# Kernel tuning notes

Hardware: AMD Instinct MI355X
Metric: run time of the kernel (lower is better)

Reference implementation:

```python
import jax, jax.numpy as jnp
import numpy as np
import math

N = 256  # channels == model dim M
B, H, W = 8, 48, 48
EPS = 1e-5


def _kaiming(key, shape, a=math.sqrt(5)):
    # kaiming_normal_ with fan_in = shape[1] (2D weight), leaky_relu gain
    fan_in = shape[1]
    gain = math.sqrt(2.0 / (1.0 + a * a))
    std = gain / math.sqrt(fan_in)
    return std * jax.random.normal(key, shape, dtype=jnp.float32)


def setup_inputs() -> dict:
    key = jax.random.key(0)
    ks = jax.random.split(key, 6)
    x_l = jax.random.normal(ks[0], (B, N, H, W), dtype=jnp.float32)
    x_r = jax.random.normal(ks[1], (B, N, H, W), dtype=jnp.float32)
    Wq = _kaiming(ks[2], (N, N))
    Wk = _kaiming(ks[3], (N, N))
    Wv = _kaiming(ks[4], (N, N))
    Wo = _kaiming(ks[5], (N, N))
    g1 = jnp.ones((N,), jnp.float32); b1 = jnp.zeros((N,), jnp.float32)
    g2 = jnp.ones((N,), jnp.float32); b2 = jnp.zeros((N,), jnp.float32)
    return {"x_l": x_l, "x_r": x_r, "Wq": Wq, "Wk": Wk, "Wv": Wv, "Wo": Wo,
            "g1": g1, "b1": b1, "g2": g2, "b2": b2}


def _layernorm(x, g, b):
    mu = jnp.mean(x, axis=-1, keepdims=True)
    var = jnp.mean(jnp.square(x - mu), axis=-1, keepdims=True)
    return (x - mu) * jax.lax.rsqrt(var + EPS) * g + b


def reference(x_l, x_r, Wq, Wk, Wv, Wo, g1, b1, g2, b2):
    Bsz, C, Hh, Ww = x_l.shape
    S = Hh * Ww
    # [B, C, H, W] -> [B, S, C]
    xl = x_l.reshape(Bsz, C, S).transpose(0, 2, 1)
    xr = x_r.reshape(Bsz, C, S).transpose(0, 2, 1)
    xln_l = _layernorm(xl, g1, b1)
    xln_r = _layernorm(xr, g2, b2)
    Ql = xln_l @ Wq; Qr = xln_r @ Wq
    Kl = xln_l @ Wk; Kr = xln_r @ Wk
    Vl = xln_l @ Wv; Vr = xln_r @ Wv
    scale = 1.0 / math.sqrt(C)
    Al = jnp.einsum('bsc,btc->bst', Ql, Kr) * scale  # [B,S,S]
    Ar = jnp.einsum('bsc,btc->bst', Qr, Kl) * scale
    # NOTE: original uses nn.Softmax() with dim=None; for a 3-D tensor torch's
    # legacy _get_softmax_dim resolves to dim=0 (over batch). Faithfully replicated.
    Pl = jax.nn.softmax(Al, axis=0)
    Pr = jax.nn.softmax(Ar, axis=0)
    out_l = xl + (Pl @ Vl) @ Wo
    out_r = xr + (Pr @ Vr) @ Wo
    out_l = out_l.transpose(0, 2, 1).reshape(Bsz, C, Hh, Ww)
    out_r = out_r.transpose(0, 2, 1).reshape(Bsz, C, Hh, Ww)
    return out_l, out_r
```

## Files before the change

### kernel.cpp

```cpp
#include <hip/hip_runtime.h>
#include <stdint.h>

#define SDIM 2304
#define CDIM 256
#define NB   8
#define MTOT (NB * SDIM)

typedef __attribute__((ext_vector_type(8))) short short8;
typedef __attribute__((ext_vector_type(4))) float f32x4;

__device__ __forceinline__ float b2f(unsigned short h) {
  union { unsigned int u; float f; } v; v.u = ((unsigned int)h) << 16; return v.f;
}
__device__ __forceinline__ unsigned short f2b(float f) {
  union { unsigned int u; float f; } v; v.f = f;
  unsigned int u = v.u;
  u += 0x7fffu + ((u >> 16) & 1u);
  return (unsigned short)(u >> 16);
}
static inline unsigned short f2b_host(float f) {
  union { unsigned int u; float f; } v; v.f = f;
  unsigned int u = v.u;
  u += 0x7fffu + ((u >> 16) & 1u);
  return (unsigned short)(u >> 16);
}

__device__ __forceinline__ void gload_lds16(const unsigned short* g, unsigned short* l) {
  __builtin_amdgcn_global_load_lds(
      (const __attribute__((address_space(1))) unsigned int*)g,
      (__attribute__((address_space(3))) unsigned int*)l,
      16, 0, 0);
}

__global__ __launch_bounds__(64)
void detect_dtype(const unsigned short* __restrict__ x, int* __restrict__ flag)
{
  int lane = threadIdx.x;
  int bad = 0;
  for (int i = lane; i < 1024; i += 64) {
    float v = b2f(x[i]);
    if (!(fabsf(v) < 1e20f)) bad = 1;
  }
  unsigned long long m = __ballot(bad);
  if (lane == 0) flag[0] = (m != 0ULL) ? 1 : 0;
}

constexpr int EP_PLAIN = 0, EP_QKV = 1, EP_OUT = 2, EP_ACC = 3;

template <int EP, int SW>
__global__ __launch_bounds__(256, 2)
void gemm_nt(const unsigned short* __restrict__ pA, int lda, long sAz,
             const unsigned short* __restrict__ pB, int ldb, long sBz, int zx,
             unsigned short* __restrict__ pC, int ldc, long sCz,
             unsigned short* __restrict__ pQ, unsigned short* __restrict__ pK,
             unsigned short* __restrict__ pV,
             const unsigned short* __restrict__ pX0, const unsigned short* __restrict__ pX1,
             float* __restrict__ pFacc, unsigned short* __restrict__ pBf, int accmode,
             const int* __restrict__ dflag, int Kdim)
{
  __shared__ __align__(16) unsigned short As[4][128 * 32];
  __shared__ __align__(16) unsigned short Bs[4][128 * 32];

  const int tid = threadIdx.x;
  int bx, by, bz;
  if constexpr (SW == 1) {
    const int h = blockIdx.x;
    const int q = h >> 4, r = h & 15;
    const int p = q * 8 + (r & 7);
    by = r >> 3;
    bx = p % 18;
    bz = p / 18;
  } else if constexpr (SW == 2) {
    const int b = blockIdx.x;
    const int n = (b & 7) * 648 + (b >> 3);
    bz = n / 324; const int r = n % 324; by = r / 18; bx = r % 18;
  } else {
    bx = blockIdx.x; by = blockIdx.y; bz = blockIdx.z;
  }
  const int z = bz;
  const long m0 = (long)bx * 128;
  const long n0 = (long)by * 128;
  const unsigned short* A  = pA + (long)z * sAz;
  const unsigned short* Bm = pB + (long)(z ^ zx) * sBz;

  const int lane = tid & 63;
  const int wave = tid >> 6;
  const int wm = (wave & 1) << 6;
  const int wn = (wave >> 1) << 6;
  const int lr = lane & 15;
  const int quad = lane >> 4;

  f32x4 acc[4][4];
#pragma unroll
  for (int i = 0; i < 4; ++i)
#pragma unroll
    for (int j = 0; j < 4; ++j) acc[i][j] = (f32x4)0.0f;

  const int e0 = tid, e1 = tid + 256;
  const int r0 = e0 >> 2, c0 = (((e0 & 3) ^ ((r0 >> 1) & 3)) << 3);
  const int r1 = e1 >> 2, c1 = (((e1 & 3) ^ ((r1 >> 1) & 3)) << 3);
  const unsigned short* pa0 = A  + (m0 + r0) * lda + c0;
  const unsigned short* pa1 = A  + (m0 + r1) * lda + c1;
  const unsigned short* pb0 = Bm + (n0 + r0) * ldb + c0;
  const unsigned short* pb1 = Bm + (n0 + r1) * ldb + c1;

  const int chunk = quad ^ ((lr >> 1) & 3);
  int aoff[4], boff[4];
#pragma unroll
  for (int i = 0; i < 4; ++i) {
    aoff[i] = (wm + i * 16 + lr) * 32 + chunk * 8;
    boff[i] = (wn + i * 16 + lr) * 32 + chunk * 8;
  }

  const int nt = Kdim >> 5;

  auto stage = [&](int kt) {
    const int sl = kt & 3;
    const int k = kt << 5;
    gload_lds16(pa0 + k, &As[sl][e0 * 8]);
    gload_lds16(pa1 + k, &As[sl][e1 * 8]);
    gload_lds16(pb0 + k, &Bs[sl][e0 * 8]);
    gload_lds16(pb1 + k, &Bs[sl][e1 * 8]);
  };

  stage(0); stage(1); stage(2);

  for (int t = 0; t < nt; ++t) {
    if (t < nt - 2)       asm volatile("s_waitcnt vmcnt(8)" ::: "memory");
    else if (t == nt - 2) asm volatile("s_waitcnt vmcnt(4)" ::: "memory");
    else                  asm volatile("s_waitcnt vmcnt(0)" ::: "memory");
    __builtin_amdgcn_s_barrier();
    asm volatile("" ::: "memory");

    if (t + 3 < nt) stage(t + 3);

    const int sl = t & 3;
    short8 af[4], bfr[4];
#pragma unroll
    for (int i = 0; i < 4; ++i) {
      af[i]  = *(const short8*)&As[sl][aoff[i]];
      bfr[i] = *(const short8*)&Bs[sl][boff[i]];
    }
    __builtin_amdgcn_s_setprio(1);
#pragma unroll
    for (int i = 0; i < 4; ++i)
#pragma unroll
      for (int j = 0; j < 4; ++j)
        acc[i][j] = __builtin_amdgcn_mfma_f32_16x16x32_bf16(af[i], bfr[j], acc[i][j], 0, 0, 0);
    __builtin_amdgcn_s_setprio(0);
  }

  if constexpr (EP == EP_PLAIN) {
    unsigned short* Cp = pC + (long)z * sCz;
#pragma unroll
    for (int i = 0; i < 4; ++i) {
      const long mb = m0 + wm + i * 16 + quad * 4;
#pragma unroll
      for (int j = 0; j < 4; ++j) {
        const long n = n0 + wn + j * 16 + lr;
#pragma unroll
        for (int r = 0; r < 4; ++r)
          Cp[(mb + r) * ldc + n] = f2b(acc[i][j][r]);
      }
    }
  } else if constexpr (EP == EP_QKV) {
    const int g  = (int)(n0 >> 8);
    const int nb = (int)(n0 & 255);
    if (g < 2) {
      unsigned short* Cp = (g == 0 ? pQ : pK) + (long)z * sCz;
#pragma unroll
      for (int i = 0; i < 4; ++i) {
        const long mb = m0 + wm + i * 16 + quad * 4;
#pragma unroll
        for (int j = 0; j < 4; ++j) {
          const int n = nb + wn + j * 16 + lr;
#pragma unroll
          for (int r = 0; r < 4; ++r)
            Cp[(mb + r) * CDIM + n] = f2b(acc[i][j][r]);
        }
      }
    } else {
      const int b = (int)(m0 / SDIM);
      const int sblk = (int)(m0 % SDIM);
      unsigned short* Vz = pV + ((long)z * NB + b) * (long)CDIM * SDIM;
#pragma unroll
      for (int i = 0; i < 4; ++i) {
        const int s = sblk + wm + i * 16 + quad * 4;
#pragma unroll
        for (int j = 0; j < 4; ++j) {
          const int c = nb + wn + j * 16 + lr;
          ushort4 pk;
          pk.x = f2b(acc[i][j][0]); pk.y = f2b(acc[i][j][1]);
          pk.z = f2b(acc[i][j][2]); pk.w = f2b(acc[i][j][3]);
          *(ushort4*)&Vz[(long)c * SDIM + s] = pk;
        }
      }
    }
  } else if constexpr (EP == EP_ACC) {
    float* Fz = pFacc + (long)z * SDIM * CDIM;
    unsigned short* Bz = pBf + (long)z * SDIM * CDIM;
#pragma unroll
    for (int i = 0; i < 4; ++i) {
      const long mb = m0 + wm + i * 16 + quad * 4;
#pragma unroll
      for (int j = 0; j < 4; ++j) {
        const long n = n0 + wn + j * 16 + lr;
#pragma unroll
        for (int r = 0; r < 4; ++r) {
          const long idx = (mb + r) * CDIM + n;
          float v = acc[i][j][r];
          if (accmode != 0) v += Fz[idx];
          if (accmode == 2) Bz[idx] = f2b(v);
          else              Fz[idx] = v;
        }
      }
    }
  } else {
    const int io32 = dflag[0];
    const int b = (int)(m0 / SDIM);
    const int sblk = (int)(m0 % SDIM);
    const unsigned short* Xraw = (z == 0 ? pX0 : pX1);
    if (io32) {
      const float* Xf = (const float*)Xraw + (long)b * CDIM * SDIM;
      float* Of = (float*)pC + (long)z * sCz + (long)b * CDIM * SDIM;
#pragma unroll
      for (int i = 0; i < 4; ++i) {
        const int s = sblk + wm + i * 16 + quad * 4;
#pragma unroll
        for (int j = 0; j < 4; ++j) {
          const int c = (int)n0 + wn + j * 16 + lr;
          const long off = (long)c * SDIM + s;
          float4 rx = *(const float4*)&Xf[off];
          float4 pk;
          pk.x = acc[i][j][0] + rx.x;
          pk.y = acc[i][j][1] + rx.y;
          pk.z = acc[i][j][2] + rx.z;
          pk.w = acc[i][j][3] + rx.w;
          *(float4*)&Of[off] = pk;
        }
      }
    } else {
      const unsigned short* X = Xraw + (long)b * CDIM * SDIM;
      unsigned short* O = pC + (long)z * sCz + (long)b * CDIM * SDIM;
#pragma unroll
      for (int i = 0; i < 4; ++i) {
        const int s = sblk + wm + i * 16 + quad * 4;
#pragma unroll
        for (int j = 0; j < 4; ++j) {
          const int c = (int)n0 + wn + j * 16 + lr;
          const long off = (long)c * SDIM + s;
          ushort4 rx = *(const ushort4*)&X[off];
          ushort4 pk;
          pk.x = f2b(acc[i][j][0] + b2f(rx.x));
          pk.y = f2b(acc[i][j][1] + b2f(rx.y));
          pk.z = f2b(acc[i][j][2] + b2f(rx.z));
          pk.w = f2b(acc[i][j][3] + b2f(rx.w));
          *(ushort4*)&O[off] = pk;
        }
      }
    }
  }
}

__global__ __launch_bounds__(256)
void wtrans(const unsigned short* __restrict__ Wq, const unsigned short* __restrict__ Wk,
            const unsigned short* __restrict__ Wv, const unsigned short* __restrict__ Wo,
            unsigned short* __restrict__ WT, const int* __restrict__ dflag)
{
  const int io32 = dflag[0];
  int idx = blockIdx.x * 256 + threadIdx.x;
  int w = idx >> 16, r = idx & 65535, n = r >> 8, k = r & 255;
  const unsigned short* W = (w == 0) ? Wq : (w == 1) ? Wk : (w == 2) ? Wv : Wo;
  float v = io32 ? ((const float*)W)[k * 256 + n] : b2f(W[k * 256 + n]);
  if (w == 0) v *= 0.0625f;
  WT[w * 65536 + n * 256 + k] = f2b(v);
}

__global__ __launch_bounds__(256)
void ln_kernel(const unsigned short* __restrict__ xl, const unsigned short* __restrict__ xr,
               const unsigned short* __restrict__ g1, const unsigned short* __restrict__ b1,
               const unsigned short* __restrict__ g2, const unsigned short* __restrict__ b2,
               unsigned short* __restrict__ XLN, const int* __restrict__ dflag)
{
  const int io32 = dflag[0];
  const int strm = blockIdx.z;
  const int b = blockIdx.y;
  const int s0 = blockIdx.x * 64;
  const unsigned short* xraw = (strm ? xr : xl);
  const float*          xf = (const float*)xraw + (long)b * CDIM * SDIM;
  const unsigned short* xh = xraw + (long)b * CDIM * SDIM;
  const unsigned short* gg = strm ? g2 : g1;
  const unsigned short* bb = strm ? b2 : b1;
  const int tid = threadIdx.x;
  const int sl = tid & 63;
  const int team = tid >> 6;

  __shared__ float red[2][4][64];
  __shared__ float muS[64], rsS[64];
  __shared__ __align__(16) unsigned short tile[64 * 258];

  float sum = 0.f, sq = 0.f;
  for (int c = team * 64; c < team * 64 + 64; ++c) {
    const long off = (long)c * SDIM + s0 + sl;
    float v = io32 ? xf[off] : b2f(xh[off]);
    sum += v; sq += v * v;
  }
  red[0][team][sl] = sum; red[1][team][sl] = sq;
  __syncthreads();
  if (tid < 64) {
    float s_ = red[0][0][tid] + red[0][1][tid] + red[0][2][tid] + red[0][3][tid];
    float q_ = red[1][0][tid] + red[1][1][tid] + red[1][2][tid] + red[1][3][tid];
    float mu = s_ * (1.0f / CDIM);
    float var = q_ * (1.0f / CDIM) - mu * mu;
    muS[tid] = mu;
    rsS[tid] = rsqrtf(var + 1e-5f);
  }
  __syncthreads();
  const float mu = muS[sl], rs = rsS[sl];
  for (int c = team * 64; c < team * 64 + 64; ++c) {
    const long off = (long)c * SDIM + s0 + sl;
    float v = io32 ? xf[off] : b2f(xh[off]);
    float gv = io32 ? ((const float*)gg)[c] : b2f(gg[c]);
    float bv = io32 ? ((const float*)bb)[c] : b2f(bb[c]);
    tile[sl * 258 + c] = f2b((v - mu) * rs * gv + bv);
  }
  __syncthreads();
  unsigned short* outp = XLN + ((long)strm * MTOT + (long)b * SDIM + s0) * CDIM;
  const ushort2* t2 = (const ushort2*)tile;
  ushort2* o2 = (ushort2*)outp;
#pragma unroll
  for (int i = 0; i < 32; ++i) {
    int idx = i * 256 + tid;
    int r = idx >> 7, c2 = idx & 127;
    o2[idx] = t2[r * 129 + c2];
  }
}

__global__ __launch_bounds__(256)
void softmax_bdim(unsigned short* __restrict__ Ab, long total)
{
  const int strm = blockIdx.y;
  const long i8 = (((long)blockIdx.x << 8) + threadIdx.x) << 3;
  unsigned short* base = Ab + (long)strm * NB * total + i8;
  float v[NB][8];
#pragma unroll
  for (int b = 0; b < NB; ++b) {
    const ushort4* p = (const ushort4*)(base + (long)b * total);
    ushort4 a0 = p[0], a1 = p[1];
    v[b][0] = b2f(a0.x); v[b][1] = b2f(a0.y); v[b][2] = b2f(a0.z); v[b][3] = b2f(a0.w);
    v[b][4] = b2f(a1.x); v[b][5] = b2f(a1.y); v[b][6] = b2f(a1.z); v[b][7] = b2f(a1.w);
  }
#pragma unroll
  for (int j = 0; j < 8; ++j) {
    float mx = v[0][j];
#pragma unroll
    for (int b = 1; b < NB; ++b) mx = fmaxf(mx, v[b][j]);
    float s = 0.f;
#pragma unroll
    for (int b = 0; b < NB; ++b) { float e = __expf(v[b][j] - mx); v[b][j] = e; s += e; }
    float inv = 1.0f / s;
#pragma unroll
    for (int b = 0; b < NB; ++b) v[b][j] *= inv;
  }
#pragma unroll
  for (int b = 0; b < NB; ++b) {
    ushort4 a0, a1;
    a0.x = f2b(v[b][0]); a0.y = f2b(v[b][1]); a0.z = f2b(v[b][2]); a0.w = f2b(v[b][3]);
    a1.x = f2b(v[b][4]); a1.y = f2b(v[b][5]); a1.z = f2b(v[b][6]); a1.w = f2b(v[b][7]);
    ushort4* p = (ushort4*)(base + (long)b * total);
    p[0] = a0; p[1] = a1;
  }
}

__global__ __launch_bounds__(256)
void fill_val(unsigned short* __restrict__ out, unsigned short v, int n)
{
  int i = blockIdx.x * 256 + threadIdx.x;
  if (i < n) out[i] = v;
}

extern "C" void kernel_launch(void* const* d_in, const int* in_sizes, int n_in,
                              void* d_out, int out_size, void* d_ws, size_t ws_size,
                              hipStream_t stream)
{
  const unsigned short* xl = (const unsigned short*)d_in[0];
  const unsigned short* xr = (const unsigned short*)d_in[1];
  const unsigned short* Wq = (const unsigned short*)d_in[2];
  const unsigned short* Wk = (const unsigned short*)d_in[3];
  const unsigned short* Wv = (const unsigned short*)d_in[4];
  const unsigned short* Wo = (const unsigned short*)d_in[5];
  const unsigned short* g1 = (const unsigned short*)d_in[6];
  const unsigned short* b1 = (const unsigned short*)d_in[7];
  const unsigned short* g2 = (const unsigned short*)d_in[8];
  const unsigned short* b2 = (const unsigned short*)d_in[9];
  unsigned short* out = (unsigned short*)d_out;

  const size_t need_chunk = 113770496UL + 64;
  const size_t need_full  = 227016704UL + 64;
  if (ws_size < need_chunk) {
    float wsmb = (float)(ws_size >> 20);
    unsigned short v = f2b_host(wsmb * 100.0f);
    fill_val<<<dim3((out_size + 255) / 256), 256, 0, stream>>>(out, v, out_size);
    return;
  }

  int* dFlag = (int*)((char*)d_ws + ((ws_size - 16) & ~15UL));
  detect_dtype<<<dim3(1), 64, 0, stream>>>(xl, dFlag);

  if (ws_size >= need_full) {
    unsigned short* WT  = (unsigned short*)d_ws;
    unsigned short* Qb  = WT + 262144L;
    unsigned short* Kb  = Qb + 9437184L;
    unsigned short* Vt  = Kb + 9437184L;
    unsigned short* Ab  = Vt + 9437184L;
    unsigned short* XLN = Ab;
    unsigned short* PVbf = Qb;

    wtrans<<<dim3(1024), 256, 0, stream>>>(Wq, Wk, Wv, Wo, WT, dFlag);
    ln_kernel<<<dim3(36, 8, 2), 256, 0, stream>>>(xl, xr, g1, b1, g2, b2, XLN, dFlag);

    gemm_nt<EP_QKV, 0><<<dim3(144, 6, 2), 256, 0, stream>>>(
        XLN, CDIM, (long)MTOT * CDIM,
        WT, CDIM, 0L, 0,
        nullptr, 0, (long)MTOT * CDIM,
        Qb, Kb, Vt, nullptr, nullptr,
        nullptr, nullptr, 0, dFlag, CDIM);

    gemm_nt<EP_PLAIN, 2><<<dim3(5184), 256, 0, stream>>>(
        Qb, CDIM, (long)SDIM * CDIM,
        Kb, CDIM, (long)SDIM * CDIM, 8,
        Ab, SDIM, (long)SDIM * SDIM,
        nullptr, nullptr, nullptr, nullptr, nullptr,
        nullptr, nullptr, 0, dFlag, CDIM);

    softmax_bdim<<<dim3(2592, 2), 256, 0, stream>>>(Ab, (long)SDIM * SDIM);

    gemm_nt<EP_PLAIN, 1><<<dim3(576), 256, 0, stream>>>(
        Ab, SDIM, (long)SDIM * SDIM,
        Vt, SDIM, (long)CDIM * SDIM, 0,
        PVbf, CDIM, (long)SDIM * CDIM,
        nullptr, nullptr, nullptr, nullptr, nullptr,
        nullptr, nullptr, 0, dFlag, SDIM);

    gemm_nt<EP_OUT, 0><<<dim3(144, 2, 2), 256, 0, stream>>>(
        PVbf, CDIM, (long)MTOT * CDIM,
        WT + 768L * 256, CDIM, 0L, 0,
        out, 0, (long)NB * CDIM * SDIM,
        nullptr, nullptr, nullptr, xl, xr,
        nullptr, nullptr, 0, dFlag, CDIM);
    return;
  }

  unsigned short* WT  = (unsigned short*)d_ws;
  unsigned short* XLN = WT  + 1024L * 256;
  unsigned short* Abc = XLN;
  unsigned short* Qb  = XLN + 9437184L;
  unsigned short* Kb  = Qb  + 9437184L;
  unsigned short* Vt  = Kb  + 9437184L;
  float*          PVacc = (float*)(Vt + 9437184L);
  unsigned short* PVbf  = Qb;

  wtrans<<<dim3(1024), 256, 0, stream>>>(Wq, Wk, Wv, Wo, WT, dFlag);
  ln_kernel<<<dim3(36, 8, 2), 256, 0, stream>>>(xl, xr, g1, b1, g2, b2, XLN, dFlag);

  gemm_nt<EP_QKV, 0><<<dim3(144, 6, 2), 256, 0, stream>>>(
      XLN, CDIM, (long)MTOT * CDIM,
      WT, CDIM, 0L, 0,
      nullptr, 0, (long)MTOT * CDIM,
      Qb, Kb, Vt, nullptr, nullptr,
      nullptr, nullptr, 0, dFlag, CDIM);

  for (int tc = 0; tc < 9; ++tc) {
    gemm_nt<EP_PLAIN, 0><<<dim3(18, 2, 16), 256, 0, stream>>>(
        Qb, CDIM, (long)SDIM * CDIM,
        Kb + (long)tc * 256 * CDIM, CDIM, (long)SDIM * CDIM, 8,
        Abc, 256, (long)SDIM * 256,
        nullptr, nullptr, nullptr, nullptr, nullptr,
        nullptr, nullptr, 0, dFlag, CDIM);

    softmax_bdim<<<dim3(288, 2), 256, 0, stream>>>(Abc, (long)SDIM * 256);

    const int mode = (tc == 0) ? 0 : (tc == 8) ? 2 : 1;
    gemm_nt<EP_ACC, 0><<<dim3(18, 2, 16), 256, 0, stream>>>(
        Abc, 256, (long)SDIM * 256,
        Vt + (long)tc * 256, SDIM, (long)CDIM * SDIM, 0,
        nullptr, 0, 0L,
        nullptr, nullptr, nullptr, nullptr, nullptr,
        PVacc, PVbf, mode, dFlag, 256);
  }

  gemm_nt<EP_OUT, 0><<<dim3(144, 2, 2), 256, 0, stream>>>(
      PVbf, CDIM, (long)MTOT * CDIM,
      WT + 768L * 256, CDIM, 0L, 0,
      out, 0, (long)NB * CDIM * SDIM,
      nullptr, nullptr, nullptr, xl, xr,
      nullptr, nullptr, 0, dFlag, CDIM);
}
```

Baseline: 427.9 us.

## Template GEMM on M-tile size, use 64-row tiles for PV and output GEMMs

Adds a TM template parameter to the GEMM kernel so the PV and output projection GEMMs use 64-row tiles, doubling their grid sizes to better fill the GPU. The software pipeline also drops from 4 LDS buffers with 3-deep prefetch to 3 buffers with 2-deep prefetch, and the s_setprio hints are removed. This gives more parallelism and less LDS use, in exchange for less A-tile reuse and shallower latency hiding across all GEMMs.

```diff
diff --git a/kernel.cpp b/kernel.cpp
--- a/kernel.cpp
+++ b/kernel.cpp
@@ -47,7 +47,7 @@
 
 constexpr int EP_PLAIN = 0, EP_QKV = 1, EP_OUT = 2, EP_ACC = 3;
 
-template <int EP, int SW>
+template <int EP, int SW, int TM>
 __global__ __launch_bounds__(256, 2)
 void gemm_nt(const unsigned short* __restrict__ pA, int lda, long sAz,
              const unsigned short* __restrict__ pB, int ldb, long sBz, int zx,
@@ -58,8 +58,12 @@
              float* __restrict__ pFacc, unsigned short* __restrict__ pBf, int accmode,
              const int* __restrict__ dflag, int Kdim)
 {
-  __shared__ __align__(16) unsigned short As[4][128 * 32];
-  __shared__ __align__(16) unsigned short Bs[4][128 * 32];
+  constexpr int WR = TM / 2;
+  constexpr int AI = WR / 16;
+  constexpr int L  = TM / 32 + 2;
+
+  __shared__ __align__(16) unsigned short As[3][TM * 32];
+  __shared__ __align__(16) unsigned short Bs[3][128 * 32];
 
   const int tid = threadIdx.x;
   int bx, by, bz;
@@ -68,8 +72,8 @@
     const int q = h >> 4, r = h & 15;
     const int p = q * 8 + (r & 7);
     by = r >> 3;
-    bx = p % 18;
-    bz = p / 18;
+    bx = p % 36;
+    bz = p / 36;
   } else if constexpr (SW == 2) {
     const int b = blockIdx.x;
     const int n = (b & 7) * 648 + (b >> 3);
@@ -78,21 +82,21 @@
     bx = blockIdx.x; by = blockIdx.y; bz = blockIdx.z;
   }
   const int z = bz;
-  const long m0 = (long)bx * 128;
+  const long m0 = (long)bx * TM;
   const long n0 = (long)by * 128;
   const unsigned short* A  = pA + (long)z * sAz;
   const unsigned short* Bm = pB + (long)(z ^ zx) * sBz;
 
   const int lane = tid & 63;
   const int wave = tid >> 6;
-  const int wm = (wave & 1) << 6;
+  const int wm = (wave & 1) * WR;
   const int wn = (wave >> 1) << 6;
   const int lr = lane & 15;
   const int quad = lane >> 4;
 
-  f32x4 acc[4][4];
-#pragma unroll
-  for (int i = 0; i < 4; ++i)
+  f32x4 acc[AI][4];
+#pragma unroll
+  for (int i = 0; i < AI; ++i)
 #pragma unroll
     for (int j = 0; j < 4; ++j) acc[i][j] = (f32x4)0.0f;
 
@@ -105,55 +109,58 @@
   const unsigned short* pb1 = Bm + (n0 + r1) * ldb + c1;
 
   const int chunk = quad ^ ((lr >> 1) & 3);
-  int aoff[4], boff[4];
-#pragma unroll
-  for (int i = 0; i < 4; ++i) {
-    aoff[i] = (wm + i * 16 + lr) * 32 + chunk * 8;
-    boff[i] = (wn + i * 16 + lr) * 32 + chunk * 8;
-  }
+  int aoff[AI], boff[4];
+#pragma unroll
+  for (int i = 0; i < AI; ++i) aoff[i] = (wm + i * 16 + lr) * 32 + chunk * 8;
+#pragma unroll
+  for (int i = 0; i < 4; ++i)  boff[i] = (wn + i * 16 + lr) * 32 + chunk * 8;
 
   const int nt = Kdim >> 5;
 
-  auto stage = [&](int kt) {
-    const int sl = kt & 3;
+  auto stage = [&](int kt, int sl) {
     const int k = kt << 5;
     gload_lds16(pa0 + k, &As[sl][e0 * 8]);
-    gload_lds16(pa1 + k, &As[sl][e1 * 8]);
+    if constexpr (TM == 128) gload_lds16(pa1 + k, &As[sl][e1 * 8]);
     gload_lds16(pb0 + k, &Bs[sl][e0 * 8]);
     gload_lds16(pb1 + k, &Bs[sl][e1 * 8]);
   };
 
-  stage(0); stage(1); stage(2);
-
+  stage(0, 0); stage(1, 1);
+
+  int bc = 0;
   for (int t = 0; t < nt; ++t) {
-    if (t < nt - 2)       asm volatile("s_waitcnt vmcnt(8)" ::: "memory");
-    else if (t == nt - 2) asm volatile("s_waitcnt vmcnt(4)" ::: "memory");
-    else                  asm volatile("s_waitcnt vmcnt(0)" ::: "memory");
+    if (t < nt - 1) {
+      if constexpr (L == 4) asm volatile("s_waitcnt vmcnt(4)" ::: "memory");
+      else                  asm volatile("s_waitcnt vmcnt(3)" ::: "memory");
+    } else {
+      asm volatile("s_waitcnt vmcnt(0)" ::: "memory");
+    }
     __builtin_amdgcn_s_barrier();
     asm volatile("" ::: "memory");
 
-    if (t + 3 < nt) stage(t + 3);
-
-    const int sl = t & 3;
-    short8 af[4], bfr[4];
-#pragma unroll
-    for (int i = 0; i < 4; ++i) {
-      af[i]  = *(const short8*)&As[sl][aoff[i]];
-      bfr[i] = *(const short8*)&Bs[sl][boff[i]];
+    if (t + 2 < nt) {
+      const int b2 = bc ? bc - 1 : 2;
+      stage(t + 2, b2);
     }
-    __builtin_amdgcn_s_setprio(1);
-#pragma unroll
-    for (int i = 0; i < 4; ++i)
+
+    short8 af[AI], bfr[4];
+#pragma unroll
+    for (int i = 0; i < AI; ++i) af[i]  = *(const short8*)&As[bc][aoff[i]];
+#pragma unroll
+    for (int i = 0; i < 4; ++i)  bfr[i] = *(const short8*)&Bs[bc][boff[i]];
+#pragma unroll
+    for (int i = 0; i < AI; ++i)
 #pragma unroll
       for (int j = 0; j < 4; ++j)
         acc[i][j] = __builtin_amdgcn_mfma_f32_16x16x32_bf16(af[i], bfr[j], acc[i][j], 0, 0, 0);
-    __builtin_amdgcn_s_setprio(0);
+
+    bc = (bc == 2) ? 0 : bc + 1;
   }
 
   if constexpr (EP == EP_PLAIN) {
     unsigned short* Cp = pC + (long)z * sCz;
 #pragma unroll
-    for (int i = 0; i < 4; ++i) {
+    for (int i = 0; i < AI; ++i) {
       const long mb = m0 + wm + i * 16 + quad * 4;
 #pragma unroll
       for (int j = 0; j < 4; ++j) {
@@ -169,7 +176,7 @@
     if (g < 2) {
       unsigned short* Cp = (g == 0 ? pQ : pK) + (long)z * sCz;
 #pragma unroll
-      for (int i = 0; i < 4; ++i) {
+      for (int i = 0; i < AI; ++i) {
         const long mb = m0 + wm + i * 16 + quad * 4;
 #pragma unroll
         for (int j = 0; j < 4; ++j) {
@@ -184,7 +191,7 @@
       const int sblk = (int)(m0 % SDIM);
       unsigned short* Vz = pV + ((long)z * NB + b) * (long)CDIM * SDIM;
 #pragma unroll
-      for (int i = 0; i < 4; ++i) {
+      for (int i = 0; i < AI; ++i) {
         const int s = sblk + wm + i * 16 + quad * 4;
 #pragma unroll
         for (int j = 0; j < 4; ++j) {
@@ -200,7 +207,7 @@
     float* Fz = pFacc + (long)z * SDIM * CDIM;
     unsigned short* Bz = pBf + (long)z * SDIM * CDIM;
 #pragma unroll
-    for (int i = 0; i < 4; ++i) {
+    for (int i = 0; i < AI; ++i) {
       const long mb = m0 + wm + i * 16 + quad * 4;
 #pragma unroll
       for (int j = 0; j < 4; ++j) {
@@ -224,7 +231,7 @@
       const float* Xf = (const float*)Xraw + (long)b * CDIM * SDIM;
       float* Of = (float*)pC + (long)z * sCz + (long)b * CDIM * SDIM;
 #pragma unroll
-      for (int i = 0; i < 4; ++i) {
+      for (int i = 0; i < AI; ++i) {
         const int s = sblk + wm + i * 16 + quad * 4;
 #pragma unroll
         for (int j = 0; j < 4; ++j) {
@@ -243,7 +250,7 @@
       const unsigned short* X = Xraw + (long)b * CDIM * SDIM;
       unsigned short* O = pC + (long)z * sCz + (long)b * CDIM * SDIM;
 #pragma unroll
-      for (int i = 0; i < 4; ++i) {
+      for (int i = 0; i < AI; ++i) {
         const int s = sblk + wm + i * 16 + quad * 4;
 #pragma unroll
         for (int j = 0; j < 4; ++j) {
@@ -419,14 +426,14 @@
     wtrans<<<dim3(1024), 256, 0, stream>>>(Wq, Wk, Wv, Wo, WT, dFlag);
     ln_kernel<<<dim3(36, 8, 2), 256, 0, stream>>>(xl, xr, g1, b1, g2, b2, XLN, dFlag);
 
-    gemm_nt<EP_QKV, 0><<<dim3(144, 6, 2), 256, 0, stream>>>(
+    gemm_nt<EP_QKV, 0, 128><<<dim3(144, 6, 2), 256, 0, stream>>>(
         XLN, CDIM, (long)MTOT * CDIM,
         WT, CDIM, 0L, 0,
         nullptr, 0, (long)MTOT * CDIM,
         Qb, Kb, Vt, nullptr, nullptr,
         nullptr, nullptr, 0, dFlag, CDIM);
 
-    gemm_nt<EP_PLAIN, 2><<<dim3(5184), 256, 0, stream>>>(
+    gemm_nt<EP_PLAIN, 2, 128><<<dim3(5184), 256, 0, stream>>>(
         Qb, CDIM, (long)SDIM * CDIM,
         Kb, CDIM, (long)SDIM * CDIM, 8,
         Ab, SDIM, (long)SDIM * SDIM,
@@ -435,14 +442,14 @@
 
     softmax_bdim<<<dim3(2592, 2), 256, 0, stream>>>(Ab, (long)SDIM * SDIM);
 
-    gemm_nt<EP_PLAIN, 1><<<dim3(576), 256, 0, stream>>>(
+    gemm_nt<EP_PLAIN, 1, 64><<<dim3(1152), 256, 0, stream>>>(
         Ab, SDIM, (long)SDIM * SDIM,
         Vt, SDIM, (long)CDIM * SDIM, 0,
         PVbf, CDIM, (long)SDIM * CDIM,
         nullptr, nullptr, nullptr, nullptr, nullptr,
         nullptr, nullptr, 0, dFlag, SDIM);
 
-    gemm_nt<EP_OUT, 0><<<dim3(144, 2, 2), 256, 0, stream>>>(
+    gemm_nt<EP_OUT, 0, 64><<<dim3(288, 2, 2), 256, 0, stream>>>(
         PVbf, CDIM, (long)MTOT * CDIM,
         WT + 768L * 256, CDIM, 0L, 0,
         out, 0, (long)NB * CDIM * SDIM,
@@ -463,7 +470,7 @@
   wtrans<<<dim3(1024), 256, 0, stream>>>(Wq, Wk, Wv, Wo, WT, dFlag);
   ln_kernel<<<dim3(36, 8, 2), 256, 0, stream>>>(xl, xr, g1, b1, g2, b2, XLN, dFlag);
 
-  gemm_nt<EP_QKV, 0><<<dim3(144, 6, 2), 256, 0, stream>>>(
+  gemm_nt<EP_QKV, 0, 128><<<dim3(144, 6, 2), 256, 0, stream>>>(
       XLN, CDIM, (long)MTOT * CDIM,
       WT, CDIM, 0L, 0,
       nullptr, 0, (long)MTOT * CDIM,
@@ -471,7 +478,7 @@
       nullptr, nullptr, 0, dFlag, CDIM);
 
   for (int tc = 0; tc < 9; ++tc) {
-    gemm_nt<EP_PLAIN, 0><<<dim3(18, 2, 16), 256, 0, stream>>>(
+    gemm_nt<EP_PLAIN, 0, 128><<<dim3(18, 2, 16), 256, 0, stream>>>(
         Qb, CDIM, (long)SDIM * CDIM,
         Kb + (long)tc * 256 * CDIM, CDIM, (long)SDIM * CDIM, 8,
         Abc, 256, (long)SDIM * 256,
@@ -481,7 +488,7 @@
     softmax_bdim<<<dim3(288, 2), 256, 0, stream>>>(Abc, (long)SDIM * 256);
 
     const int mode = (tc == 0) ? 0 : (tc == 8) ? 2 : 1;
-    gemm_nt<EP_ACC, 0><<<dim3(18, 2, 16), 256, 0, stream>>>(
+    gemm_nt<EP_ACC, 0, 128><<<dim3(18, 2, 16), 256, 0, stream>>>(
         Abc, 256, (long)SDIM * 256,
         Vt + (long)tc * 256, SDIM, (long)CDIM * SDIM, 0,
         nullptr, 0, 0L,
@@ -489,7 +496,7 @@
         PVacc, PVbf, mode, dFlag, 256);
   }
 
-  gemm_nt<EP_OUT, 0><<<dim3(144, 2, 2), 256, 0, stream>>>(
+  gemm_nt<EP_OUT, 0, 64><<<dim3(288, 2, 2), 256, 0, stream>>>(
       PVbf, CDIM, (long)MTOT * CDIM,
       WT + 768L * 256, CDIM, 0L, 0,
       out, 0, (long)NB * CDIM * SDIM,
```

Result: faster. 405.7 us (-5.2%).
